# Optimization experiments

Hardware: AMD Instinct MI355X
Metric: run time of the kernel (lower is better)

Reference implementation:

```python
import jax, jax.numpy as jnp
import numpy as np

D_IN = 1024
D_OUT = 1024
N_HEADS = 16
D_HEAD = D_OUT // N_HEADS


def setup_inputs() -> dict:
    key = jax.random.key(0)
    ks = jax.random.split(key, 6)
    s = 0.02
    return {
        "x": jax.random.normal(ks[0], (4, 2048, D_IN), dtype=jnp.float32),
        "wq": jax.random.normal(ks[1], (D_IN, D_OUT), dtype=jnp.float32) * s,
        "wk": jax.random.normal(ks[2], (D_IN, D_OUT), dtype=jnp.float32) * s,
        "wv": jax.random.normal(ks[3], (D_IN, D_OUT), dtype=jnp.float32) * s,
        "wo": jax.random.normal(ks[4], (D_OUT, D_OUT), dtype=jnp.float32) * s,
        "bo": jax.random.normal(ks[5], (D_OUT,), dtype=jnp.float32) * s,
    }


def reference(x, wq, wk, wv, wo, bo):
    B, T, _ = x.shape
    # QKV projections (no bias), split into heads: (B, H, T, Dh)
    def split_heads(t):
        return t.reshape(B, T, N_HEADS, D_HEAD).transpose(0, 2, 1, 3)
    q = split_heads(x @ wq)
    k = split_heads(x @ wk)
    v = split_heads(x @ wv)
    # attention scores (B, H, T, T), causal mask, scale by sqrt(d_head)
    scores = jnp.einsum("bhqd,bhkd->bhqk", q, k)
    causal = jnp.tril(jnp.ones((T, T), dtype=bool))
    scores = jnp.where(causal, scores, -jnp.inf)
    attn = jax.nn.softmax(scores / jnp.sqrt(jnp.float32(D_HEAD)), axis=-1)
    # dropout = 0.0 (eval) -> identity
    ctx = jnp.einsum("bhqk,bhkd->bhqd", attn, v)
    ctx = ctx.transpose(0, 2, 1, 3).reshape(B, T, D_OUT)
    return ctx @ wo + bo
```

## Files before the change

kernel.cpp:

```cpp
#include <hip/hip_runtime.h>
#include <stdint.h>


typedef unsigned short u16;
typedef __bf16 bf16x8 __attribute__((ext_vector_type(8)));
typedef short s16x4 __attribute__((ext_vector_type(4)));
typedef float f32x4 __attribute__((ext_vector_type(4)));

__device__ __forceinline__ u16 f2bf(float f) {
  union { float f; unsigned u; } v; v.f = f;
  return (u16)((v.u + 0x7fffu + ((v.u >> 16) & 1u)) >> 16);
}

__device__ __forceinline__ void gl_lds16(const void* g, void* l) {
  __builtin_amdgcn_global_load_lds((__attribute__((address_space(1))) void*)g,
                                   (__attribute__((address_space(3))) void*)l,
                                   16, 0, 0);
}

__global__ __launch_bounds__(256) void conv_x_k(const float* __restrict__ x,
                                                u16* __restrict__ xb) {
  int i = (blockIdx.x * 256 + threadIdx.x) * 4;
  float4 v = *reinterpret_cast<const float4*>(x + i);
  ushort4 o;
  o.x = f2bf(v.x); o.y = f2bf(v.y); o.z = f2bf(v.z); o.w = f2bf(v.w);
  *reinterpret_cast<ushort4*>(xb + i) = o;
}

__global__ __launch_bounds__(256) void conv_w_k(const float* __restrict__ w0,
                                                const float* __restrict__ w1,
                                                const float* __restrict__ w2,
                                                const float* __restrict__ w3,
                                                u16* __restrict__ dst) {
  const float* src = blockIdx.z == 0 ? w0 : blockIdx.z == 1 ? w1
                   : blockIdx.z == 2 ? w2 : w3;
  u16* d = dst + (size_t)blockIdx.z * 1024 * 1024;
  __shared__ float tile[32][33];
  int n0 = blockIdx.x * 32, k0 = blockIdx.y * 32;
  int tx = threadIdx.x & 31, ty = threadIdx.x >> 5;
  #pragma unroll
  for (int r = 0; r < 32; r += 8)
    tile[ty + r][tx] = src[(k0 + ty + r) * 1024 + n0 + tx];
  __syncthreads();
  #pragma unroll
  for (int r = 0; r < 32; r += 8)
    d[(n0 + ty + r) * 1024 + k0 + tx] = f2bf(tile[tx][ty + r]);
}

#define SWZ128(row, chunk) ((row) * 128 + ((((chunk) ^ ((row) & 7))) << 4))

__global__ __launch_bounds__(256) void gemm_qkv_k(const u16* __restrict__ A,
                                                  const u16* __restrict__ Wt,
                                                  u16* __restrict__ qw,
                                                  u16* __restrict__ kw,
                                                  u16* __restrict__ vtw) {
  __shared__ u16 SM[32768];
  const int tid = threadIdx.x;
  const int wave = tid >> 6, lane = tid & 63;
  const int quad = lane >> 4, l15 = lane & 15;
  const int m0 = blockIdx.x * 128;
  const int which = blockIdx.y >> 3;
  const int n0 = (blockIdx.y & 7) * 128;
  const u16* Bt = Wt + which * (1024 * 1024);
  const int waveM = (wave >> 1) * 64, waveN = (wave & 1) * 64;

  const f32x4 fz = {0.f, 0.f, 0.f, 0.f};
  f32x4 acc[4][4];
  #pragma unroll
  for (int i = 0; i < 4; i++)
    #pragma unroll
    for (int j = 0; j < 4; j++) acc[i][j] = fz;

  const int lrow8 = lane >> 3, lchunk = lane & 7;
  const int gsw = (lchunk ^ lrow8) * 8;
  const u16* Agp[4];
  const u16* Bgp[4];
  #pragma unroll
  for (int i = 0; i < 4; i++) {
    Agp[i] = A + (m0 + i * 32 + wave * 8 + lrow8) * 1024 + gsw;
    Bgp[i] = Bt + (n0 + i * 32 + wave * 8 + lrow8) * 1024 + gsw;
  }

  #pragma unroll
  for (int i = 0; i < 4; i++) {
    gl_lds16(Agp[i], (char*)SM + i * 4096 + wave * 1024);
    gl_lds16(Bgp[i], (char*)SM + 32768 + i * 4096 + wave * 1024);
  }

  #pragma unroll
  for (int s = 0; s < 16; s++) {
    const int o = (s & 1) * 16384;
    __syncthreads();
    if (s < 15) {
      const int nxt = 16384 - o;
      const int koff = (s + 1) * 64;
      #pragma unroll
      for (int i = 0; i < 4; i++) {
        gl_lds16(Agp[i] + koff, (char*)SM + nxt + i * 4096 + wave * 1024);
        gl_lds16(Bgp[i] + koff, (char*)SM + 32768 + nxt + i * 4096 + wave * 1024);
      }
    }
    #pragma unroll
    for (int kk = 0; kk < 2; kk++) {
      bf16x8 af[4], bf[4];
      #pragma unroll
      for (int mi = 0; mi < 4; mi++)
        af[mi] = *reinterpret_cast<const bf16x8*>(
            (char*)SM + o + SWZ128(waveM + mi * 16 + l15, kk * 4 + quad));
      #pragma unroll
      for (int ni = 0; ni < 4; ni++)
        bf[ni] = *reinterpret_cast<const bf16x8*>(
            (char*)SM + 32768 + o + SWZ128(waveN + ni * 16 + l15, kk * 4 + quad));
      #pragma unroll
      for (int mi = 0; mi < 4; mi++)
        #pragma unroll
        for (int ni = 0; ni < 4; ni++)
          acc[mi][ni] = __builtin_amdgcn_mfma_f32_16x16x32_bf16(af[mi], bf[ni], acc[mi][ni], 0, 0, 0);
    }
  }

  if (which != 2) {
    #pragma unroll
    for (int mi = 0; mi < 4; mi++) {
      #pragma unroll
      for (int r = 0; r < 4; r++) {
        int m = m0 + waveM + mi * 16 + quad * 4 + r;
        int b = m >> 11, t = m & 2047;
        #pragma unroll
        for (int ni = 0; ni < 4; ni++) {
          int n = n0 + waveN + ni * 16 + l15;
          int h = n >> 6, d = n & 63;
          float v = acc[mi][ni][r];
          if (which == 0) qw[((b * 16 + h) * 2048 + t) * 64 + d] = f2bf(v * 0.125f);
          else            kw[((b * 16 + h) * 2048 + t) * 64 + d] = f2bf(v);
        }
      }
    }
  } else {
    __syncthreads();
    #pragma unroll
    for (int mi = 0; mi < 4; mi++)
      #pragma unroll
      for (int r = 0; r < 4; r++) {
        int ml = waveM + mi * 16 + quad * 4 + r;
        #pragma unroll
        for (int ni = 0; ni < 4; ni++) {
          int nl = waveN + ni * 16 + l15;
          int byte = nl * 256 + (((ml >> 3) ^ (nl & 7)) << 4) + (ml & 7) * 2;
          *(u16*)((char*)SM + byte) = f2bf(acc[mi][ni][r]);
        }
      }
    __syncthreads();
    const int b = m0 >> 11, t0 = m0 & 2047;
    #pragma unroll
    for (int i = 0; i < 8; i++) {
      int cid = tid + 256 * i;
      int nl = cid >> 4, tc = cid & 15;
      bf16x8 vv = *reinterpret_cast<const bf16x8*>(
          (char*)SM + nl * 256 + ((tc ^ (nl & 7)) << 4));
      int n = n0 + nl;
      int h = n >> 6, d = n & 63;
      *reinterpret_cast<bf16x8*>(vtw + (((b * 16 + h) * 64 + d) * 2048 + t0 + tc * 8)) = vv;
    }
  }
}

__global__ __launch_bounds__(256) void attn_k(const u16* __restrict__ Q,
                                              const u16* __restrict__ K,
                                              const u16* __restrict__ Vt,
                                              u16* __restrict__ ctx) {
  __shared__ u16 Qs[64 * 64];
  __shared__ u16 Ks[2][64 * 64];
  __shared__ u16 Vs[2][64 * 64];
  const int tid = threadIdx.x;
  const int wave = tid >> 6, lane = tid & 63;
  const int quad = lane >> 4, l15 = lane & 15;
  const int bh = blockIdx.x;
  const int qt = 31 - (int)blockIdx.y;
  const int b = bh >> 4, h = bh & 15;

  const u16* Qg = Q + (bh * 2048 + qt * 64) * 64;
  const u16* Kg = K + bh * (2048 * 64);
  const u16* Vg = Vt + bh * (64 * 2048);

  const int lrow = tid >> 3;
  const int lsw = ((tid & 7) ^ (lrow & 7)) * 8;

  gl_lds16(Qg + lrow * 64 + lsw, (char*)Qs + wave * 1024);
  gl_lds16(Qg + (32 + lrow) * 64 + lsw, (char*)Qs + wave * 1024 + 4096);
  {
    char* KsB = (char*)Ks[0] + wave * 1024;
    char* VsB = (char*)Vs[0] + wave * 1024;
    gl_lds16(Kg + lrow * 64 + lsw, KsB);
    gl_lds16(Kg + (32 + lrow) * 64 + lsw, KsB + 4096);
    gl_lds16(Vg + lrow * 2048 + lsw, VsB);
    gl_lds16(Vg + (32 + lrow) * 2048 + lsw, VsB + 4096);
  }

  const s16x4 ones4 = {(short)0x3F80, (short)0x3F80, (short)0x3F80, (short)0x3F80};
  const f32x4 fz = {0.f, 0.f, 0.f, 0.f};
  f32x4 accO[4];
  f32x4 accL = fz;
  #pragma unroll
  for (int dt = 0; dt < 4; dt++) accO[dt] = fz;
  bf16x8 qf[2];

  #define SWZB(row, chunk) ((row) * 128 + (((chunk) ^ ((row) & 7)) << 4))

  for (int j = 0; j <= qt; j++) {
    const int cur = j & 1;
    __syncthreads();
    if (j < qt) {
      char* KsB = (char*)Ks[cur ^ 1] + wave * 1024;
      char* VsB = (char*)Vs[cur ^ 1] + wave * 1024;
      const int jr = (j + 1) * 64;
      gl_lds16(Kg + (jr + lrow) * 64 + lsw, KsB);
      gl_lds16(Kg + (jr + 32 + lrow) * 64 + lsw, KsB + 4096);
      gl_lds16(Vg + lrow * 2048 + jr + lsw, VsB);
      gl_lds16(Vg + (32 + lrow) * 2048 + jr + lsw, VsB + 4096);
    }
    if (j == 0) {
      #pragma unroll
      for (int kk = 0; kk < 2; kk++)
        qf[kk] = *reinterpret_cast<const bf16x8*>(
            (char*)Qs + SWZB(wave * 16 + l15, kk * 4 + quad));
    }

    f32x4 s[4];
    #pragma unroll
    for (int nt = 0; nt < 4; nt++) s[nt] = fz;
    #pragma unroll
    for (int kk = 0; kk < 2; kk++)
      #pragma unroll
      for (int nt = 0; nt < 4; nt++) {
        bf16x8 kf = *reinterpret_cast<const bf16x8*>(
            (char*)Ks[cur] + SWZB(nt * 16 + l15, kk * 4 + quad));
        s[nt] = __builtin_amdgcn_mfma_f32_16x16x32_bf16(kf, qf[kk], s[nt], 0, 0, 0);
      }

    if (j == qt) {
      const int qrow = wave * 16 + l15;
      #pragma unroll
      for (int nt = 0; nt < 4; nt++)
        #pragma unroll
        for (int r = 0; r < 4; r++)
          if (nt * 16 + quad * 4 + r > qrow) s[nt][r] = -1e30f;
    }

    s16x4 pf[4];
    #pragma unroll
    for (int nt = 0; nt < 4; nt++) {
      float p0 = __expf(s[nt][0]), p1 = __expf(s[nt][1]);
      float p2 = __expf(s[nt][2]), p3 = __expf(s[nt][3]);
      union { s16x4 v; unsigned u[2]; } pk;
      pk.u[0] = __builtin_amdgcn_perm(__float_as_uint(p1), __float_as_uint(p0),
                                      0x07060302u);
      pk.u[1] = __builtin_amdgcn_perm(__float_as_uint(p3), __float_as_uint(p2),
                                      0x07060302u);
      pf[nt] = pk.v;
    }

    #pragma unroll
    for (int kc = 0; kc < 4; kc++) {
      accL = __builtin_amdgcn_mfma_f32_16x16x16bf16_1k(pf[kc], ones4, accL, 0, 0, 0);
      #pragma unroll
      for (int dt = 0; dt < 4; dt++) {
        int row = dt * 16 + l15;
        int byte = row * 128 + (((kc * 2 + (quad >> 1)) ^ (l15 & 7)) << 4) +
                   (quad & 1) * 8;
        s16x4 vf = *reinterpret_cast<const s16x4*>((char*)Vs[cur] + byte);
        accO[dt] = __builtin_amdgcn_mfma_f32_16x16x16bf16_1k(pf[kc], vf, accO[dt], 0, 0, 0);
      }
    }
  }
  #undef SWZB

  float inv[4];
  #pragma unroll
  for (int r = 0; r < 4; r++) inv[r] = 1.0f / accL[r];
  const int trow = qt * 64 + wave * 16 + quad * 4;
  #pragma unroll
  for (int dt = 0; dt < 4; dt++)
    #pragma unroll
    for (int r = 0; r < 4; r++)
      ctx[(b * 2048 + trow + r) * 1024 + h * 64 + dt * 16 + l15] =
          f2bf(accO[dt][r] * inv[r]);
}

__global__ __launch_bounds__(256) void gemm_out_k(const u16* __restrict__ A,
                                                  const u16* __restrict__ Wt,
                                                  const float* __restrict__ bo,
                                                  float* __restrict__ out) {
  __shared__ u16 SM[32768];
  const int tid = threadIdx.x;
  const int wave = tid >> 6, lane = tid & 63;
  const int quad = lane >> 4, l15 = lane & 15;
  const int m0 = blockIdx.x * 128;
  const int n0 = blockIdx.y * 128;
  const int waveM = (wave >> 1) * 64, waveN = (wave & 1) * 64;

  const f32x4 fz = {0.f, 0.f, 0.f, 0.f};
  f32x4 acc[4][4];
  #pragma unroll
  for (int i = 0; i < 4; i++)
    #pragma unroll
    for (int j = 0; j < 4; j++) acc[i][j] = fz;

  const int lrow8 = lane >> 3, lchunk = lane & 7;
  const int gsw = (lchunk ^ lrow8) * 8;
  const u16* Agp[4];
  const u16* Bgp[4];
  #pragma unroll
  for (int i = 0; i < 4; i++) {
    Agp[i] = A + (m0 + i * 32 + wave * 8 + lrow8) * 1024 + gsw;
    Bgp[i] = Wt + (n0 + i * 32 + wave * 8 + lrow8) * 1024 + gsw;
  }

  #pragma unroll
  for (int i = 0; i < 4; i++) {
    gl_lds16(Agp[i], (char*)SM + i * 4096 + wave * 1024);
    gl_lds16(Bgp[i], (char*)SM + 32768 + i * 4096 + wave * 1024);
  }

  #pragma unroll
  for (int s = 0; s < 16; s++) {
    const int o = (s & 1) * 16384;
    __syncthreads();
    if (s < 15) {
      const int nxt = 16384 - o;
      const int koff = (s + 1) * 64;
      #pragma unroll
      for (int i = 0; i < 4; i++) {
        gl_lds16(Agp[i] + koff, (char*)SM + nxt + i * 4096 + wave * 1024);
        gl_lds16(Bgp[i] + koff, (char*)SM + 32768 + nxt + i * 4096 + wave * 1024);
      }
    }
    #pragma unroll
    for (int kk = 0; kk < 2; kk++) {
      bf16x8 af[4], bf[4];
      #pragma unroll
      for (int mi = 0; mi < 4; mi++)
        af[mi] = *reinterpret_cast<const bf16x8*>(
            (char*)SM + o + SWZ128(waveM + mi * 16 + l15, kk * 4 + quad));
      #pragma unroll
      for (int ni = 0; ni < 4; ni++)
        bf[ni] = *reinterpret_cast<const bf16x8*>(
            (char*)SM + 32768 + o + SWZ128(waveN + ni * 16 + l15, kk * 4 + quad));
      #pragma unroll
      for (int mi = 0; mi < 4; mi++)
        #pragma unroll
        for (int ni = 0; ni < 4; ni++)
          acc[mi][ni] = __builtin_amdgcn_mfma_f32_16x16x32_bf16(af[mi], bf[ni], acc[mi][ni], 0, 0, 0);
    }
  }
  float bias[4];
  #pragma unroll
  for (int ni = 0; ni < 4; ni++) bias[ni] = bo[n0 + waveN + ni * 16 + l15];
  #pragma unroll
  for (int mi = 0; mi < 4; mi++)
    #pragma unroll
    for (int r = 0; r < 4; r++) {
      int m = m0 + waveM + mi * 16 + quad * 4 + r;
      #pragma unroll
      for (int ni = 0; ni < 4; ni++) {
        int n = n0 + waveN + ni * 16 + l15;
        out[(size_t)m * 1024 + n] = acc[mi][ni][r] + bias[ni];
      }
    }
}

extern "C" void kernel_launch(void* const* d_in, const int* in_sizes, int n_in,
                              void* d_out, int out_size, void* d_ws, size_t ws_size,
                              hipStream_t stream) {
  const float* x  = (const float*)d_in[0];
  const float* wq = (const float*)d_in[1];
  const float* wk = (const float*)d_in[2];
  const float* wv = (const float*)d_in[3];
  const float* wo = (const float*)d_in[4];
  const float* bo = (const float*)d_in[5];
  float* out = (float*)d_out;
  char* ws = (char*)d_ws;

  u16* xb  = (u16*)(ws);
  u16* wt  = (u16*)(ws + 16777216);
  u16* qw  = (u16*)(ws + 25165824);
  u16* kw  = (u16*)(ws + 41943040);
  u16* vtw = (u16*)(ws + 58720256);

  conv_x_k<<<8192, 256, 0, stream>>>(x, xb);
  conv_w_k<<<dim3(32, 32, 4), 256, 0, stream>>>(wq, wk, wv, wo, wt);
  gemm_qkv_k<<<dim3(64, 24), 256, 0, stream>>>(xb, wt, qw, kw, vtw);
  attn_k<<<dim3(64, 32), 256, 0, stream>>>(qw, kw, vtw, xb );
  gemm_out_k<<<dim3(64, 8), 256, 0, stream>>>(xb, wt + 3 * 1024 * 1024, bo, out);
}
```

Baseline: 231.8 us.

## Use native exp2 with log2e-folded Q scale and permute V^T layout for wide LDS reads

```diff
diff --git a/kernel.cpp b/kernel.cpp
--- a/kernel.cpp
+++ b/kernel.cpp
@@ -6,6 +6,8 @@
 typedef __bf16 bf16x8 __attribute__((ext_vector_type(8)));
 typedef short s16x4 __attribute__((ext_vector_type(4)));
 typedef float f32x4 __attribute__((ext_vector_type(4)));
+
+extern "C" __device__ float __ocml_native_exp2_f32(float);
 
 __device__ __forceinline__ u16 f2bf(float f) {
   union { float f; unsigned u; } v; v.f = f;
@@ -131,7 +133,7 @@
           int n = n0 + waveN + ni * 16 + l15;
           int h = n >> 6, d = n & 63;
           float v = acc[mi][ni][r];
-          if (which == 0) qw[((b * 16 + h) * 2048 + t) * 64 + d] = f2bf(v * 0.125f);
+          if (which == 0) qw[((b * 16 + h) * 2048 + t) * 64 + d] = f2bf(v * 0.18033688f);
           else            kw[((b * 16 + h) * 2048 + t) * 64 + d] = f2bf(v);
         }
       }
@@ -156,11 +158,19 @@
     for (int i = 0; i < 8; i++) {
       int cid = tid + 256 * i;
       int nl = cid >> 4, tc = cid & 15;
-      bf16x8 vv = *reinterpret_cast<const bf16x8*>(
-          (char*)SM + nl * 256 + ((tc ^ (nl & 7)) << 4));
+      int tb = tc >> 3, cp = tc & 7;
+      int gl = ((2 * cp) & 3) * 4 + ((2 * cp) >> 2);
+      int gh = ((2 * cp + 1) & 3) * 4 + ((2 * cp + 1) >> 2);
+      int ml0 = tb * 64 + gl * 4, ml1 = tb * 64 + gh * 4;
+      s16x4 lo = *reinterpret_cast<const s16x4*>(
+          (char*)SM + nl * 256 + (((ml0 >> 3) ^ (nl & 7)) << 4) + (ml0 & 7) * 2);
+      s16x4 hi = *reinterpret_cast<const s16x4*>(
+          (char*)SM + nl * 256 + (((ml1 >> 3) ^ (nl & 7)) << 4) + (ml1 & 7) * 2);
+      union { s16x4 hh[2]; bf16x8 w; } uu;
+      uu.hh[0] = lo; uu.hh[1] = hi;
       int n = n0 + nl;
       int h = n >> 6, d = n & 63;
-      *reinterpret_cast<bf16x8*>(vtw + (((b * 16 + h) * 64 + d) * 2048 + t0 + tc * 8)) = vv;
+      *reinterpret_cast<bf16x8*>(vtw + (((b * 16 + h) * 64 + d) * 2048 + t0 + tc * 8)) = uu.w;
     }
   }
 }
@@ -250,8 +260,10 @@
     s16x4 pf[4];
     #pragma unroll
     for (int nt = 0; nt < 4; nt++) {
-      float p0 = __expf(s[nt][0]), p1 = __expf(s[nt][1]);
-      float p2 = __expf(s[nt][2]), p3 = __expf(s[nt][3]);
+      float p0 = __ocml_native_exp2_f32(s[nt][0]);
+      float p1 = __ocml_native_exp2_f32(s[nt][1]);
+      float p2 = __ocml_native_exp2_f32(s[nt][2]);
+      float p3 = __ocml_native_exp2_f32(s[nt][3]);
       union { s16x4 v; unsigned u[2]; } pk;
       pk.u[0] = __builtin_amdgcn_perm(__float_as_uint(p1), __float_as_uint(p0),
                                       0x07060302u);
@@ -260,17 +272,22 @@
       pf[nt] = pk.v;
     }
 
+    union { bf16x8 w; s16x4 hh[2]; } vv[2][4];
+    #pragma unroll
+    for (int r2 = 0; r2 < 2; r2++)
+      #pragma unroll
+      for (int dt = 0; dt < 4; dt++) {
+        int row = dt * 16 + l15;
+        vv[r2][dt].w = *reinterpret_cast<const bf16x8*>(
+            (char*)Vs[cur] + row * 128 + (((quad * 2 + r2) ^ (row & 7)) << 4));
+      }
     #pragma unroll
     for (int kc = 0; kc < 4; kc++) {
       accL = __builtin_amdgcn_mfma_f32_16x16x16bf16_1k(pf[kc], ones4, accL, 0, 0, 0);
       #pragma unroll
-      for (int dt = 0; dt < 4; dt++) {
-        int row = dt * 16 + l15;
-        int byte = row * 128 + (((kc * 2 + (quad >> 1)) ^ (l15 & 7)) << 4) +
-                   (quad & 1) * 8;
-        s16x4 vf = *reinterpret_cast<const s16x4*>((char*)Vs[cur] + byte);
-        accO[dt] = __builtin_amdgcn_mfma_f32_16x16x16bf16_1k(pf[kc], vf, accO[dt], 0, 0, 0);
-      }
+      for (int dt = 0; dt < 4; dt++)
+        accO[dt] = __builtin_amdgcn_mfma_f32_16x16x16bf16_1k(
+            pf[kc], vv[kc >> 1][dt].hh[kc & 1], accO[dt], 0, 0, 0);
     }
   }
   #undef SWZB
```

Result: no change. 230.8 us (-0.4%).
